# Performance work log

Hardware: AMD Instinct MI355X
Metric: run time of the kernel (lower is better)

The kernel has to match this reference:

```python
import jax, jax.numpy as jnp
from jax import lax
import numpy as np

D_MODEL = 256
NQ = 256          # nqueries / npoint
RADIUS = 0.3
NSAMPLE = 16
EPS = 1e-5


def _conv1d(x, W, b):  # x: (B,C,N), W: (O,C)
    return jnp.einsum('bcn,oc->bon', x, W) + b[None, :, None]


def _bn1d(x, g, be):  # train-mode batchnorm over (B, N)
    m = x.mean(axis=(0, 2), keepdims=True)
    v = x.var(axis=(0, 2), keepdims=True)
    return g[None, :, None] * (x - m) * lax.rsqrt(v + EPS) + be[None, :, None]


def _bn2d(x, g, be):  # x: (B,C,Q,S)
    m = x.mean(axis=(0, 2, 3), keepdims=True)
    v = x.var(axis=(0, 2, 3), keepdims=True)
    return g[None, :, None, None] * (x - m) * lax.rsqrt(v + EPS) + be[None, :, None, None]


def _fps(xyz, nq):
    # sequential farthest point sampling, starts at index 0 (matches CUDA impl)
    B, N, _ = xyz.shape

    def step(carry, _):
        dist, far = carry
        centroid = jnp.take_along_axis(xyz, far[:, None, None], axis=1)  # (B,1,3)
        d = jnp.sum((xyz - centroid) ** 2, axis=-1)                      # (B,N)
        dist = jnp.minimum(dist, d)
        nxt = jnp.argmax(dist, axis=-1).astype(jnp.int32)
        return (dist, nxt), far

    init = (jnp.full((B, N), 1e10, xyz.dtype), jnp.zeros((B,), jnp.int32))
    _, inds = lax.scan(step, init, None, length=nq)
    return inds.T  # (B,nq)


def _ball_query(query_xyz, xyz, radius, nsample):
    # query_xyz: (B,Q,3), xyz: (B,N,3) -> idx (B,Q,nsample) int32
    N = xyz.shape[1]
    d2 = jnp.sum((query_xyz[:, :, None, :] - xyz[:, None, :, :]) ** 2, axis=-1)  # (B,Q,N)
    within = d2 < radius * radius
    scores = jnp.where(within, jnp.arange(N, dtype=jnp.int32), jnp.int32(N))
    neg_top, _ = lax.top_k(-scores, nsample)          # nsample smallest scores, in order
    idx = -neg_top                                    # (B,Q,nsample)
    cnt = within.sum(axis=-1)                         # (B,Q)
    first = jnp.where(cnt > 0, idx[..., 0], 0)        # fill value (first neighbor, else 0)
    valid = jnp.arange(nsample) < cnt[..., None]
    return jnp.where(valid, idx, first[..., None])


def setup_inputs() -> dict:
    key = jax.random.key(0)
    ks = jax.random.split(key, 32)
    B, N, C = 16, 4096, D_MODEL
    s = 0.02
    inp = {
        'encode_xyz': jax.random.uniform(ks[0], (B, N, 3), jnp.float32),
        'encode_features': jax.random.normal(ks[1], (B, C, N), jnp.float32),
        # FFN_vote: conv1 -> bn -> relu -> conv2 -> bn -> relu -> conv3
        'W1': jax.random.normal(ks[2], (C, C), jnp.float32) * s,
        'b1': jnp.zeros((C,), jnp.float32),
        'g1': jnp.ones((C,), jnp.float32),
        'be1': jnp.zeros((C,), jnp.float32),
        'W2': jax.random.normal(ks[3], (C, C), jnp.float32) * s,
        'b2': jnp.zeros((C,), jnp.float32),
        'g2': jnp.ones((C,), jnp.float32),
        'be2': jnp.zeros((C,), jnp.float32),
        'W3': jax.random.normal(ks[4], (3 + C, C), jnp.float32) * s,
        'b3': jnp.zeros((3 + C,), jnp.float32),
        # SA module shared MLP (conv2d 1x1): (C+3)->C->C->C, each with BN2d
        'mW1': jax.random.normal(ks[5], (C, C + 3), jnp.float32) * s,
        'mb1': jnp.zeros((C,), jnp.float32),
        'mg1': jnp.ones((C,), jnp.float32),
        'mbe1': jnp.zeros((C,), jnp.float32),
        'mW2': jax.random.normal(ks[6], (C, C), jnp.float32) * s,
        'mb2': jnp.zeros((C,), jnp.float32),
        'mg2': jnp.ones((C,), jnp.float32),
        'mbe2': jnp.zeros((C,), jnp.float32),
        'mW3': jax.random.normal(ks[7], (C, C), jnp.float32) * s,
        'mb3': jnp.zeros((C,), jnp.float32),
        'mg3': jnp.ones((C,), jnp.float32),
        'mbe3': jnp.zeros((C,), jnp.float32),
    }
    return inp


def reference(encode_xyz, encode_features, W1, b1, g1, be1, W2, b2, g2, be2, W3, b3,
              mW1, mb1, mg1, mbe1, mW2, mb2, mg2, mbe2, mW3, mb3, mg3, mbe3):
    B, N, _ = encode_xyz.shape

    # FFN_vote
    h = jax.nn.relu(_bn1d(_conv1d(encode_features, W1, b1), g1, be1))
    h = jax.nn.relu(_bn1d(_conv1d(h, W2, b2), g2, be2))
    out = _conv1d(h, W3, b3)                      # (B, 3+C, N)

    coord_shift = jnp.clip(jax.nn.sigmoid(out[:, :3, :]), 0.1, 0.9)
    vote_xyz = encode_xyz + coord_shift.transpose(0, 2, 1) - 0.5   # (B,N,3)

    feat = encode_features + out[:, 3:, :]
    feat = feat / jnp.linalg.norm(feat, axis=1, keepdims=True)     # L2 normalize over C

    sample_inds = _fps(encode_xyz, NQ)                             # (B,NQ) int32

    # SA module: gather new centers from vote_xyz at FPS inds
    query_xyz = jnp.take_along_axis(vote_xyz, sample_inds[:, :, None], axis=1)  # (B,NQ,3)

    idx = _ball_query(query_xyz, vote_xyz, RADIUS, NSAMPLE)        # (B,NQ,NS)
    bidx = jnp.arange(B)[:, None, None]
    grouped_xyz = (vote_xyz[bidx, idx] - query_xyz[:, :, None, :]) / RADIUS  # (B,NQ,NS,3)
    grouped_feat = feat.transpose(0, 2, 1)[bidx, idx]                         # (B,NQ,NS,C)
    g = jnp.concatenate([grouped_xyz, grouped_feat], axis=-1)                 # (B,NQ,NS,3+C)
    g = g.transpose(0, 3, 1, 2)                                               # (B,3+C,NQ,NS)

    g = jax.nn.relu(_bn2d(jnp.einsum('bcqs,oc->boqs', g, mW1) + mb1[None, :, None, None], mg1, mbe1))
    g = jax.nn.relu(_bn2d(jnp.einsum('bcqs,oc->boqs', g, mW2) + mb2[None, :, None, None], mg2, mbe2))
    g = jax.nn.relu(_bn2d(jnp.einsum('bcqs,oc->boqs', g, mW3) + mb3[None, :, None, None], mg3, mbe3))
    query_features = jnp.max(g, axis=-1)                                      # (B,C,NQ)

    return vote_xyz, encode_xyz, sample_inds, query_xyz, query_features
```

## Files before the change

kernel.cpp:

```cpp
#include <hip/hip_runtime.h>
#include <math.h>

#define NPT 4096
#define NB 16

typedef short v8s __attribute__((ext_vector_type(8)));
typedef float v4f __attribute__((ext_vector_type(4)));

__device__ __forceinline__ float dist2e(float x, float y, float z,
                                        float cx, float cy, float cz) {
    float dx = __fsub_rn(x, cx), dy = __fsub_rn(y, cy), dz = __fsub_rn(z, cz);
    return __fadd_rn(__fadd_rn(__fmul_rn(dx, dx), __fmul_rn(dy, dy)), __fmul_rn(dz, dz));
}

__device__ __forceinline__ unsigned long long packdi(float v, int n) {
    return ((unsigned long long)__float_as_uint(v) << 32) |
           (unsigned long long)(0xFFFFFFFFu - (unsigned)n);
}

__device__ __forceinline__ unsigned short f2bf(float f) {
    unsigned u = __float_as_uint(f);
    u = u + 0x7FFFu + ((u >> 16) & 1u);
    return (unsigned short)(u >> 16);
}

__device__ __forceinline__ unsigned pk2(float a, float b) {
    unsigned r;
    asm("v_cvt_pk_bf16_f32 %0, %1, %2" : "=v"(r) : "v"(a), "v"(b));
    return r;
}

__device__ __forceinline__ uint2 split2(float a, float b) {
    unsigned h = pk2(a, b);
    float ra = __uint_as_float(h << 16);
    float rb = __uint_as_float(h & 0xFFFF0000u);
    unsigned l = pk2(a - ra, b - rb);
    return make_uint2(h, l);
}

__device__ void fps_seg(const float* __restrict__ xyz, int b, int it0, int it1,
                        int* __restrict__ inds_i, float* __restrict__ inds_f,
                        float* __restrict__ dws, int* __restrict__ farws,
                        char* scr) {
    float (*s_cent)[3] = (float (*)[3])scr;
    unsigned long long (*s_red)[4] = (unsigned long long (*)[4])(scr + 32);
    const int t = threadIdx.x;
    const int lane = t & 63, wid = t >> 6;
    const float* pb = xyz + (size_t)b * NPT * 3;
    float px[16], py[16], pz[16], d[16];
    #pragma unroll
    for (int j = 0; j < 16; ++j) {
        int p = j * 256 + t;
        px[j] = pb[p * 3 + 0];
        py[j] = pb[p * 3 + 1];
        pz[j] = pb[p * 3 + 2];
    }
    int far;
    if (it0 == 0) {
        #pragma unroll
        for (int j = 0; j < 16; ++j) d[j] = 1e10f;
        far = 0;
    } else {
        #pragma unroll
        for (int j = 0; j < 16; ++j) d[j] = dws[b * 4096 + j * 256 + t];
        far = farws[b];
    }
    for (int it = it0; it < it1; ++it) {
        const int par = it & 1;
        if (t == 0) { inds_i[it] = far; inds_f[it] = (float)far; }
        if (t == (far & 255)) {
            const int jj = far >> 8;
            float cx = px[0], cy = py[0], cz = pz[0];
            #pragma unroll
            for (int j = 1; j < 16; ++j)
                if (j == jj) { cx = px[j]; cy = py[j]; cz = pz[j]; }
            s_cent[par][0] = cx; s_cent[par][1] = cy; s_cent[par][2] = cz;
        }
        __syncthreads();
        const float cx = s_cent[par][0], cy = s_cent[par][1], cz = s_cent[par][2];
        d[0] = fminf(d[0], dist2e(px[0], py[0], pz[0], cx, cy, cz));
        unsigned long long best = packdi(d[0], t);
        #pragma unroll
        for (int j = 1; j < 16; ++j) {
            d[j] = fminf(d[j], dist2e(px[j], py[j], pz[j], cx, cy, cz));
            unsigned long long c = packdi(d[j], j * 256 + t);
            if (c > best) best = c;
        }
        #pragma unroll
        for (int s = 32; s; s >>= 1) {
            unsigned long long o = __shfl_down(best, (unsigned)s, 64);
            if (o > best) best = o;
        }
        if (lane == 0) s_red[par][wid] = best;
        __syncthreads();
        unsigned long long m = s_red[par][0];
        if (s_red[par][1] > m) m = s_red[par][1];
        if (s_red[par][2] > m) m = s_red[par][2];
        if (s_red[par][3] > m) m = s_red[par][3];
        far = (int)(0xFFFFFFFFu - (unsigned)(m & 0xFFFFFFFFull));
    }
    if (it1 < 256) {
        #pragma unroll
        for (int j = 0; j < 16; ++j) dws[b * 4096 + j * 256 + t] = d[j];
        if (t == 0) farws[b] = far;
    }
}

template <bool PRE_BN, bool STATS>
__global__ __launch_bounds__(256, 2)
void fgemm_k(const float* __restrict__ X,
             const unsigned short* __restrict__ Wh,
             const unsigned short* __restrict__ Wl,
             const float* __restrict__ bias,
             const float* __restrict__ scl, const float* __restrict__ sft,
             float* __restrict__ Y,
             float* __restrict__ psum, float* __restrict__ psqr,
             const float* __restrict__ xyz, int* __restrict__ sinds,
             float* __restrict__ inds_f, float* __restrict__ fpsd,
             int* __restrict__ fpsfar, int it0, int it1) {
    __shared__ __align__(16) unsigned short sAh[128 * 64];
    __shared__ __align__(16) unsigned short sAl[128 * 64];
    __shared__ __align__(16) unsigned short sBh[128 * 64];
    __shared__ __align__(16) unsigned short sBl[128 * 64];
    if (blockIdx.x < 16) {
        fps_seg(xyz, blockIdx.x, it0, it1, sinds + blockIdx.x * 256,
                inds_f + blockIdx.x * 256, fpsd, fpsfar, (char*)sAh);
        return;
    }
    int idx = blockIdx.x - 16;
    idx = (idx & 7) * 128 + (idx >> 3);
    const int b = idx >> 6, rem = idx & 63;
    const int nt = rem >> 1;
    const int n0 = nt * 128, o0 = (rem & 1) * 128;
    const int t = threadIdx.x;
    const int w = t >> 6, lane = t & 63;
    const int wm = (w >> 1) * 64, wn = (w & 1) * 64;
    const int lr = lane & 15, lk = lane >> 4;
    char* cAh = (char*)sAh; char* cAl = (char*)sAl;
    char* cBh = (char*)sBh; char* cBl = (char*)sBl;

    v4f acc[4][4];
    v4f zz = {0.f, 0.f, 0.f, 0.f};
    #pragma unroll
    for (int i = 0; i < 4; ++i)
        #pragma unroll
        for (int j = 0; j < 4; ++j) acc[i][j] = zz;

    const int ra = t >> 1, kb2 = (t & 1) * 64;
    const unsigned short* ah = Wh + (size_t)(o0 + ra) * 256 + (t & 1) * 32;
    const unsigned short* al = Wl + (size_t)(o0 + ra) * 256 + (t & 1) * 32;
    const int swA = (ra & 7) << 4;
    const int cblk = t >> 5, nq = t & 31;
    const float* xb = X + ((size_t)b * 256 + cblk * 8) * 4096 + n0 + nq * 4;

    #pragma unroll 1
    for (int ks = 0; ks < 4; ++ks) {
        const int k0 = ks * 64;
        uint4 avh[4], avl[4];
        #pragma unroll
        for (int i = 0; i < 4; ++i) {
            avh[i] = *(const uint4*)(ah + k0 + 8 * i);
            avl[i] = *(const uint4*)(al + k0 + 8 * i);
        }
        v4f xv[8];
        #pragma unroll
        for (int i = 0; i < 8; ++i)
            xv[i] = *(const v4f*)(xb + (size_t)(k0 + i) * 4096);
        if (PRE_BN) {
            const v4f s0 = *(const v4f*)(scl + k0 + cblk * 8);
            const v4f s1 = *(const v4f*)(scl + k0 + cblk * 8 + 4);
            const v4f f0 = *(const v4f*)(sft + k0 + cblk * 8);
            const v4f f1 = *(const v4f*)(sft + k0 + cblk * 8 + 4);
            #pragma unroll
            for (int i = 0; i < 8; ++i) {
                const float si = (i < 4) ? s0[i] : s1[i - 4];
                const float fi = (i < 4) ? f0[i] : f1[i - 4];
                #pragma unroll
                for (int j = 0; j < 4; ++j)
                    xv[i][j] = fmaxf(fmaf(xv[i][j], si, fi), 0.f);
            }
        }
        __syncthreads();
        #pragma unroll
        for (int i = 0; i < 4; ++i) {
            *(uint4*)(cAh + ra * 128 + ((kb2 + 16 * i) ^ swA)) = avh[i];
            *(uint4*)(cAl + ra * 128 + ((kb2 + 16 * i) ^ swA)) = avl[i];
        }
        #pragma unroll
        for (int j = 0; j < 4; ++j) {
            const int n = nq * 4 + j;
            uint2 p0 = split2(xv[0][j], xv[1][j]);
            uint2 p1 = split2(xv[2][j], xv[3][j]);
            uint2 p2 = split2(xv[4][j], xv[5][j]);
            uint2 p3 = split2(xv[6][j], xv[7][j]);
            uint4 hh, ll;
            hh.x = p0.x; hh.y = p1.x; hh.z = p2.x; hh.w = p3.x;
            ll.x = p0.y; ll.y = p1.y; ll.z = p2.y; ll.w = p3.y;
            const int ad = n * 128 + ((cblk * 16) ^ ((n & 7) << 4));
            *(uint4*)(cBh + ad) = hh;
            *(uint4*)(cBl + ad) = ll;
        }
        __syncthreads();
        #pragma unroll
        for (int kb = 0; kb < 2; ++kb) {
            const int koff = kb * 64 + lk * 16;
            v8s ahf[4], alf[4], bhf[4], blf[4];
            #pragma unroll
            for (int f = 0; f < 4; ++f) {
                const int rm = wm + f * 16 + lr;
                const int am = rm * 128 + (koff ^ ((rm & 7) << 4));
                ahf[f] = *(const v8s*)(cAh + am);
                alf[f] = *(const v8s*)(cAl + am);
                const int rn = wn + f * 16 + lr;
                const int bm = rn * 128 + (koff ^ ((rn & 7) << 4));
                bhf[f] = *(const v8s*)(cBh + bm);
                blf[f] = *(const v8s*)(cBl + bm);
            }
            #pragma unroll
            for (int fm = 0; fm < 4; ++fm)
                #pragma unroll
                for (int fn = 0; fn < 4; ++fn) {
                    acc[fm][fn] = __builtin_amdgcn_mfma_f32_16x16x32_bf16(
                        ahf[fm], bhf[fn], acc[fm][fn], 0, 0, 0);
                    acc[fm][fn] = __builtin_amdgcn_mfma_f32_16x16x32_bf16(
                        ahf[fm], blf[fn], acc[fm][fn], 0, 0, 0);
                    acc[fm][fn] = __builtin_amdgcn_mfma_f32_16x16x32_bf16(
                        alf[fm], bhf[fn], acc[fm][fn], 0, 0, 0);
                }
        }
    }

    float* Yb = Y + (size_t)b * 256 * 4096;
    const int gnt = b * 32 + nt;
    #pragma unroll
    for (int fm = 0; fm < 4; ++fm) {
        const int obase = o0 + wm + fm * 16 + lk * 4;
        float bv[4];
        #pragma unroll
        for (int j = 0; j < 4; ++j) bv[j] = bias[obase + j];
        float ssr[4] = {0.f, 0.f, 0.f, 0.f}, qqr[4] = {0.f, 0.f, 0.f, 0.f};
        #pragma unroll
        for (int fn = 0; fn < 4; ++fn) {
            const int gn = n0 + wn + fn * 16 + lr;
            #pragma unroll
            for (int j = 0; j < 4; ++j) {
                const float yv = acc[fm][fn][j] + bv[j];
                Yb[(size_t)(obase + j) * 4096 + gn] = yv;
                ssr[j] += yv; qqr[j] += yv * yv;
            }
        }
        if (STATS) {
            #pragma unroll
            for (int j = 0; j < 4; ++j) {
                #pragma unroll
                for (int off = 1; off < 16; off <<= 1) {
                    ssr[j] += __shfl_xor(ssr[j], off, 64);
                    qqr[j] += __shfl_xor(qqr[j], off, 64);
                }
            }
            if (lr == 0) {
                const int col = gnt * 2 + (w & 1);
                #pragma unroll
                for (int j = 0; j < 4; ++j) {
                    psum[(size_t)(obase + j) * 1024 + col] = ssr[j];
                    psqr[(size_t)(obase + j) * 1024 + col] = qqr[j];
                }
            }
        }
    }
}

__global__ __launch_bounds__(256)
void prepw_k(const float* __restrict__ W1, const float* __restrict__ W2,
             const float* __restrict__ W3, unsigned short* __restrict__ h1,
             unsigned short* __restrict__ l1, unsigned short* __restrict__ h2,
             unsigned short* __restrict__ l2, unsigned short* __restrict__ h3,
             unsigned short* __restrict__ l3) {
    const int o = blockIdx.x & 255, which = blockIdx.x >> 8, t = threadIdx.x;
    float v;
    unsigned short* ph;
    unsigned short* pl;
    if (which == 0) { v = W1[(size_t)o * 256 + t]; ph = h1; pl = l1; }
    else if (which == 1) { v = W2[(size_t)o * 256 + t]; ph = h2; pl = l2; }
    else { v = W3[(size_t)(o + 3) * 256 + t]; ph = h3; pl = l3; }
    unsigned short hu = f2bf(v);
    float rv = v - __uint_as_float((unsigned)hu << 16);
    ph[o * 256 + t] = hu;
    pl[o * 256 + t] = f2bf(rv);
}

__global__ __launch_bounds__(64)
void fin_k(const float* __restrict__ psum, const float* __restrict__ psqr,
           const float* __restrict__ g, const float* __restrict__ be,
           float* __restrict__ scl, float* __restrict__ sft, int npart) {
    const int c = blockIdx.x, t = threadIdx.x;
    const float4* ps = (const float4*)(psum + (size_t)c * 1024);
    const float4* pq = (const float4*)(psqr + (size_t)c * 1024);
    float s = 0.f, q = 0.f;
    for (int r = t; r < (npart >> 2); r += 64) {
        float4 a = ps[r]; s += a.x + a.y + a.z + a.w;
        float4 b2 = pq[r]; q += b2.x + b2.y + b2.z + b2.w;
    }
    #pragma unroll
    for (int sh = 32; sh; sh >>= 1) {
        s += __shfl_down(s, (unsigned)sh, 64);
        q += __shfl_down(q, (unsigned)sh, 64);
    }
    if (t == 0) {
        float mean = s * (1.f / 65536.f);
        float var = q * (1.f / 65536.f) - mean * mean;
        float sc = g[c] / sqrtf(var + 1e-5f);
        scl[c] = sc;
        sft[c] = be[c] - mean * sc;
    }
}

__global__ __launch_bounds__(256)
void prep_k(const float* __restrict__ mW1, const float* __restrict__ mW2,
            const float* __restrict__ mW3, unsigned short* __restrict__ W1p,
            unsigned short* __restrict__ W2p, unsigned short* __restrict__ W3p) {
    const int o = blockIdx.x & 255, which = blockIdx.x >> 8, t = threadIdx.x;
    if (which == 0) {
        W1p[o * 320 + t] = f2bf(mW1[o * 259 + 3 + t]);
        if (t < 64) {
            float v = (t < 3) ? mW1[o * 259 + t] : 0.f;
            W1p[o * 320 + 256 + t] = f2bf(v);
        }
    } else if (which == 1) {
        W2p[o * 256 + t] = f2bf(mW2[o * 256 + t]);
    } else {
        W3p[o * 256 + t] = f2bf(mW3[o * 256 + t]);
    }
}

__global__ __launch_bounds__(256)
void votefeat_k(const float* __restrict__ OUT, const float* __restrict__ Y2,
                const float* __restrict__ xyz, const float* __restrict__ feats,
                const float* __restrict__ scl2, const float* __restrict__ sft2,
                const float* __restrict__ W3, const float* __restrict__ b3,
                float* __restrict__ vote_out, float* __restrict__ xyz_out,
                unsigned short* __restrict__ featT) {
    const int blk = blockIdx.x;
    const int b = blk >> 7, n0 = (blk & 127) * 32;
    const int t = threadIdx.x;
    __shared__ float tile[32 * 257];
    __shared__ float ssb[32 * 9];
    __shared__ float rn[32];
    __shared__ float sW3[768];
    __shared__ float dred[3][8][33];
    const int nl = t & 31, co = t >> 5;
    const float* Ob = OUT + (size_t)b * 256 * NPT;
    const float* Yb = Y2 + (size_t)b * 256 * NPT;
    #pragma unroll
    for (int r = 0; r < 3; ++r) sW3[r * 256 + t] = W3[r * 256 + t];
    __syncthreads();
    float ss = 0.f, d0 = 0.f, d1 = 0.f, d2 = 0.f;
    #pragma unroll 4
    for (int ci = 0; ci < 32; ++ci) {
        const int c = ci * 8 + co;
        const size_t coff = (size_t)c * NPT + n0 + nl;
        float v = feats[(size_t)b * 256 * NPT + coff] + Ob[coff];
        tile[nl * 257 + c] = v;
        ss += v * v;
        float h = fmaxf(fmaf(Yb[coff], scl2[c], sft2[c]), 0.f);
        d0 = fmaf(h, sW3[c], d0);
        d1 = fmaf(h, sW3[256 + c], d1);
        d2 = fmaf(h, sW3[512 + c], d2);
    }
    ssb[nl * 9 + co] = ss;
    dred[0][co][nl] = d0;
    dred[1][co][nl] = d1;
    dred[2][co][nl] = d2;
    __syncthreads();
    if (t < 32) {
        float s = 0.f;
        #pragma unroll
        for (int j = 0; j < 8; ++j) s += ssb[t * 9 + j];
        rn[t] = 1.0f / sqrtf(s);
    }
    __syncthreads();
    for (int p = 0; p < 32; ++p)
        featT[((size_t)b * NPT + n0 + p) * 256 + t] = f2bf(tile[p * 257 + t] * rn[p]);
    if (t < 96) {
        const int r = t >> 5, p = t & 31;
        float d = b3[r];
        #pragma unroll
        for (int j = 0; j < 8; ++j) d += dred[r][j][p];
        float sig = 1.f / (1.f + expf(-d));
        sig = fminf(fmaxf(sig, 0.1f), 0.9f);
        const size_t gi = ((size_t)b * NPT + n0 + p) * 3 + r;
        const float e = xyz[gi];
        vote_out[gi] = e + sig - 0.5f;
        xyz_out[gi] = e;
    }
}

__global__ __launch_bounds__(64)
void bq_k(const float* __restrict__ vote, const int* __restrict__ sinds,
          float* __restrict__ qxyz_out, int* __restrict__ idx_out) {
    const int bq = blockIdx.x;
    const int b = bq >> 8;
    const int lane = threadIdx.x;
    __shared__ int s_idx[16];
    const int si = sinds[bq];
    const float* vb = vote + (size_t)b * NPT * 3;
    const float qx = vb[si * 3 + 0], qy = vb[si * 3 + 1], qz = vb[si * 3 + 2];
    if (lane < 3) qxyz_out[bq * 3 + lane] = vb[si * 3 + lane];
    int cnt = 0;
    for (int cb = 0; cb < 64 && cnt < 16; ++cb) {
        int n = cb * 64 + lane;
        float x = vb[n * 3], y = vb[n * 3 + 1], z = vb[n * 3 + 2];
        float d2 = dist2e(x, y, z, qx, qy, qz);
        unsigned long long m = __ballot(d2 < 0.09f);
        while (m && cnt < 16) {
            int bit = __builtin_ctzll(m);
            s_idx[cnt] = cb * 64 + bit;
            ++cnt;
            m &= m - 1;
        }
    }
    __syncthreads();
    if (lane < 16) {
        int v = (lane < cnt) ? s_idx[lane] : (cnt > 0 ? s_idx[0] : 0);
        idx_out[bq * 16 + lane] = v;
    }
}

__global__ __launch_bounds__(256)
void group_k(const unsigned short* __restrict__ featT, const float* __restrict__ vote,
             const float* __restrict__ qxyz, const int* __restrict__ idxs,
             unsigned short* __restrict__ Gt) {
    const int bq = blockIdx.x;
    const int b = bq >> 8, q = bq & 255;
    const int t = threadIdx.x;
    __shared__ int s_i[16];
    __shared__ float s_q[3];
    if (t < 16) s_i[t] = idxs[bq * 16 + t];
    if (t < 3) s_q[t] = qxyz[bq * 3 + t];
    __syncthreads();
    const int s = t >> 4, part = t & 15;
    const int i = s_i[s];
    const size_t nrow = (size_t)b * 4096 + q * 16 + s;
    const uint4* src = (const uint4*)(featT + ((size_t)b * NPT + i) * 256 + part * 16);
    uint4* dst = (uint4*)(Gt + nrow * 320 + part * 16);
    dst[0] = src[0];
    dst[1] = src[1];
    for (int c = 259 + part; c < 320; c += 16) Gt[nrow * 320 + c] = 0;
    if (part < 3) {
        float v = (vote[((size_t)b * NPT + i) * 3 + part] - s_q[part]) * (1.f / 0.3f);
        Gt[nrow * 320 + 256 + part] = f2bf(v);
    }
}

__device__ __forceinline__ unsigned bnpair(unsigned u, float sl, float sh,
                                           float fl, float fh) {
    float lo = __uint_as_float(u << 16);
    float hi = __uint_as_float(u & 0xFFFF0000u);
    lo = fmaxf(fmaf(lo, sl, fl), 0.f);
    hi = fmaxf(fmaf(hi, sh, fh), 0.f);
    unsigned r;
    asm("v_cvt_pk_bf16_f32 %0, %1, %2" : "=v"(r) : "v"(lo), "v"(hi));
    return r;
}

template <int KPAD, bool BNSTAGE, bool EPIMAX>
__global__ __launch_bounds__(256, 2)
void mgemm_k(const unsigned short* __restrict__ Wb,
             const unsigned short* __restrict__ Xt,
             const float* __restrict__ bias,
             const float* __restrict__ scl, const float* __restrict__ sft,
             unsigned short* __restrict__ Yt, float* __restrict__ rmax,
             float* __restrict__ psum, float* __restrict__ psqr) {
    __shared__ __align__(16) unsigned short sA[128 * 64];
    __shared__ __align__(16) unsigned short sB[128 * 64];
    char* cA = (char*)sA;
    char* cB = (char*)sB;
    const int t = threadIdx.x;
    const int n0 = blockIdx.x * 128, o0 = blockIdx.y * 128;
    const int w = t >> 6, lane = t & 63;
    const int wm = (w >> 1) * 64, wn = (w & 1) * 64;
    const int lr = lane & 15, lk = lane >> 4;

    v4f acc[4][4];
    v4f zz = {0.f, 0.f, 0.f, 0.f};
    #pragma unroll
    for (int i = 0; i < 4; ++i)
        #pragma unroll
        for (int j = 0; j < 4; ++j) acc[i][j] = zz;

    const int ra = t >> 1, kc = (t & 1) * 32;
    const unsigned short* asrc = Wb + (size_t)(o0 + ra) * KPAD + kc;
    const unsigned short* bsrc = Xt + (size_t)(n0 + ra) * KPAD + kc;
    const int nk = KPAD / 64;

    for (int ks = 0; ks < nk; ++ks) {
        const int k0 = ks * 64;
        uint4 av[4], bv[4];
        #pragma unroll
        for (int i = 0; i < 4; ++i) av[i] = *(const uint4*)(asrc + k0 + 8 * i);
        #pragma unroll
        for (int i = 0; i < 4; ++i) bv[i] = *(const uint4*)(bsrc + k0 + 8 * i);
        if constexpr (BNSTAGE) {
            #pragma unroll
            for (int i = 0; i < 4; ++i) {
                const int kk = k0 + kc + 8 * i;
                float4 s0 = *(const float4*)(scl + kk);
                float4 s1 = *(const float4*)(scl + kk + 4);
                float4 f0 = *(const float4*)(sft + kk);
                float4 f1 = *(const float4*)(sft + kk + 4);
                bv[i].x = bnpair(bv[i].x, s0.x, s0.y, f0.x, f0.y);
                bv[i].y = bnpair(bv[i].y, s0.z, s0.w, f0.z, f0.w);
                bv[i].z = bnpair(bv[i].z, s1.x, s1.y, f1.x, f1.y);
                bv[i].w = bnpair(bv[i].w, s1.z, s1.w, f1.z, f1.w);
            }
        }
        __syncthreads();
        #pragma unroll
        for (int i = 0; i < 4; ++i) {
            const int kb2 = (kc + 8 * i) * 2;
            *(uint4*)(cA + ra * 128 + (kb2 ^ ((ra & 7) << 4))) = av[i];
            *(uint4*)(cB + ra * 128 + (kb2 ^ ((ra & 7) << 4))) = bv[i];
        }
        __syncthreads();
        #pragma unroll
        for (int kb = 0; kb < 2; ++kb) {
            const int koff = (kb * 32 + lk * 8) * 2;
            v8s af[4], bf[4];
            #pragma unroll
            for (int f = 0; f < 4; ++f) {
                const int rm = wm + f * 16 + lr;
                af[f] = *(const v8s*)(cA + rm * 128 + (koff ^ ((rm & 7) << 4)));
                const int rn = wn + f * 16 + lr;
                bf[f] = *(const v8s*)(cB + rn * 128 + (koff ^ ((rn & 7) << 4)));
            }
            #pragma unroll
            for (int fm = 0; fm < 4; ++fm)
                #pragma unroll
                for (int fn = 0; fn < 4; ++fn)
                    acc[fm][fn] = __builtin_amdgcn_mfma_f32_16x16x32_bf16(
                        af[fm], bf[fn], acc[fm][fn], 0, 0, 0);
        }
    }

    const int bx = blockIdx.x;
    #pragma unroll
    for (int fm = 0; fm < 4; ++fm) {
        const int obase = o0 + wm + fm * 16 + lk * 4;
        const float4 bv4 = *(const float4*)(bias + obase);
        float s0 = 0.f, s1 = 0.f, s2 = 0.f, s3 = 0.f;
        float q0 = 0.f, q1 = 0.f, q2 = 0.f, q3 = 0.f;
        #pragma unroll
        for (int fn = 0; fn < 4; ++fn) {
            float y0 = acc[fm][fn][0] + bv4.x;
            float y1 = acc[fm][fn][1] + bv4.y;
            float y2 = acc[fm][fn][2] + bv4.z;
            float y3 = acc[fm][fn][3] + bv4.w;
            s0 += y0; s1 += y1; s2 += y2; s3 += y3;
            q0 += y0 * y0; q1 += y1 * y1; q2 += y2 * y2; q3 += y3 * y3;
            if constexpr (!EPIMAX) {
                unsigned p0, p1;
                asm("v_cvt_pk_bf16_f32 %0, %1, %2" : "=v"(p0) : "v"(y0), "v"(y1));
                asm("v_cvt_pk_bf16_f32 %0, %1, %2" : "=v"(p1) : "v"(y2), "v"(y3));
                const int gn = n0 + wn + fn * 16 + lr;
                *(uint2*)(Yt + (size_t)gn * 256 + obase) = make_uint2(p0, p1);
            } else {
                float m0 = y0, m1 = y1, m2 = y2, m3 = y3;
                #pragma unroll
                for (int off = 1; off < 16; off <<= 1) {
                    m0 = fmaxf(m0, __shfl_xor(m0, off, 64));
                    m1 = fmaxf(m1, __shfl_xor(m1, off, 64));
                    m2 = fmaxf(m2, __shfl_xor(m2, off, 64));
                    m3 = fmaxf(m3, __shfl_xor(m3, off, 64));
                }
                if (lr == 0) {
                    const int gq = (n0 + wn + fn * 16) >> 4;
                    const int bb = gq >> 8, qq = gq & 255;
                    float* rp = rmax + ((size_t)bb * 256 + obase) * 256 + qq;
                    rp[0] = m0; rp[256] = m1; rp[512] = m2; rp[768] = m3;
                }
            }
        }
        #pragma unroll
        for (int off = 1; off < 16; off <<= 1) {
            s0 += __shfl_xor(s0, off, 64); q0 += __shfl_xor(q0, off, 64);
            s1 += __shfl_xor(s1, off, 64); q1 += __shfl_xor(q1, off, 64);
            s2 += __shfl_xor(s2, off, 64); q2 += __shfl_xor(q2, off, 64);
            s3 += __shfl_xor(s3, off, 64); q3 += __shfl_xor(q3, off, 64);
        }
        if (lr == 0) {
            const int col = bx * 2 + (w & 1);
            psum[(size_t)(obase + 0) * 1024 + col] = s0;
            psum[(size_t)(obase + 1) * 1024 + col] = s1;
            psum[(size_t)(obase + 2) * 1024 + col] = s2;
            psum[(size_t)(obase + 3) * 1024 + col] = s3;
            psqr[(size_t)(obase + 0) * 1024 + col] = q0;
            psqr[(size_t)(obase + 1) * 1024 + col] = q1;
            psqr[(size_t)(obase + 2) * 1024 + col] = q2;
            psqr[(size_t)(obase + 3) * 1024 + col] = q3;
        }
    }
}

__global__ __launch_bounds__(256)
void qf_k(const float* __restrict__ rmax, const float* __restrict__ scl,
          const float* __restrict__ sft, float* __restrict__ out) {
    const int g = blockIdx.x * 256 + threadIdx.x;
    const int c = (g >> 8) & 255;
    out[g] = fmaxf(fmaf(rmax[g], scl[c], sft[c]), 0.f);
}

extern "C" void kernel_launch(void* const* d_in, const int* in_sizes, int n_in,
                              void* d_out, int out_size, void* d_ws, size_t ws_size,
                              hipStream_t stream) {
    const float* xyz   = (const float*)d_in[0];
    const float* feats = (const float*)d_in[1];
    const float* W1 = (const float*)d_in[2];
    const float* b1 = (const float*)d_in[3];
    const float* g1 = (const float*)d_in[4];
    const float* be1 = (const float*)d_in[5];
    const float* W2 = (const float*)d_in[6];
    const float* b2 = (const float*)d_in[7];
    const float* g2 = (const float*)d_in[8];
    const float* be2 = (const float*)d_in[9];
    const float* W3 = (const float*)d_in[10];
    const float* b3 = (const float*)d_in[11];
    const float* mW1 = (const float*)d_in[12];
    const float* mb1 = (const float*)d_in[13];
    const float* mg1 = (const float*)d_in[14];
    const float* mbe1 = (const float*)d_in[15];
    const float* mW2 = (const float*)d_in[16];
    const float* mb2 = (const float*)d_in[17];
    const float* mg2 = (const float*)d_in[18];
    const float* mbe2 = (const float*)d_in[19];
    const float* mW3 = (const float*)d_in[20];
    const float* mb3 = (const float*)d_in[21];
    const float* mg3 = (const float*)d_in[22];
    const float* mbe3 = (const float*)d_in[23];

    float* out_vote = (float*)d_out;
    float* out_xyz = out_vote + 196608;
    float* out_inds = out_xyz + 196608;
    float* out_q = out_inds + 4096;
    float* out_qf = out_q + 12288;

    float* ws = (float*)d_ws;
    float* A      = ws;
    float* Bb     = A + 16973824;
    float* Ft     = Bb + 16777216;
    float* rawmax = Ft + 8388608;
    float* psum   = rawmax + 1048576;
    float* psqr   = psum + 262144;
    float* st     = psqr + 262144;
    float* fpsd   = st + 2560;
    float* wbase  = fpsd + 65536;
    unsigned short* Wb1 = (unsigned short*)wbase;
    unsigned short* Wb2 = Wb1 + 81920;
    unsigned short* Wb3 = Wb2 + 65536;
    int* sinds  = (int*)(Wb3 + 65536);
    int* bidx   = sinds + 4096;
    int* fpsfar = bidx + 65536;

    unsigned short* Gt  = (unsigned short*)A;
    unsigned short* Y1t = (unsigned short*)Bb;
    unsigned short* featT = (unsigned short*)Ft;
    unsigned short* Y2t = (unsigned short*)Ft;

    unsigned short* Wf1h = (unsigned short*)rawmax;
    unsigned short* Wf1l = Wf1h + 65536;
    unsigned short* Wf2h = Wf1l + 65536;
    unsigned short* Wf2l = Wf2h + 65536;
    unsigned short* Wf3h = Wf2l + 65536;
    unsigned short* Wf3l = Wf3h + 65536;

    prep_k<<<768, 256, 0, stream>>>(mW1, mW2, mW3, Wb1, Wb2, Wb3);
    prepw_k<<<768, 256, 0, stream>>>(W1, W2, W3, Wf1h, Wf1l, Wf2h, Wf2l, Wf3h, Wf3l);

    fgemm_k<false, true><<<1040, 256, 0, stream>>>(
        feats, Wf1h, Wf1l, b1, nullptr, nullptr, A, psum, psqr,
        xyz, sinds, out_inds, fpsd, fpsfar, 0, 86);
    fin_k<<<256, 64, 0, stream>>>(psum, psqr, g1, be1, st + 0, st + 256, 1024);
    fgemm_k<true, true><<<1040, 256, 0, stream>>>(
        A, Wf2h, Wf2l, b2, st + 0, st + 256, Bb, psum, psqr,
        xyz, sinds, out_inds, fpsd, fpsfar, 86, 172);
    fin_k<<<256, 64, 0, stream>>>(psum, psqr, g2, be2, st + 512, st + 768, 1024);
    fgemm_k<true, false><<<1040, 256, 0, stream>>>(
        Bb, Wf3h, Wf3l, b3 + 3, st + 512, st + 768, A, nullptr, nullptr,
        xyz, sinds, out_inds, fpsd, fpsfar, 172, 256);

    votefeat_k<<<2048, 256, 0, stream>>>(A, Bb, xyz, feats, st + 512, st + 768,
                                         W3, b3, out_vote, out_xyz, featT);
    bq_k<<<4096, 64, 0, stream>>>(out_vote, sinds, out_q, bidx);
    group_k<<<4096, 256, 0, stream>>>(featT, out_vote, out_q, bidx, Gt);

    mgemm_k<320, false, false><<<dim3(512, 2), 256, 0, stream>>>(
        Wb1, Gt, mb1, nullptr, nullptr, Y1t, nullptr, psum, psqr);
    fin_k<<<256, 64, 0, stream>>>(psum, psqr, mg1, mbe1, st + 1024, st + 1280, 1024);
    mgemm_k<256, true, false><<<dim3(512, 2), 256, 0, stream>>>(
        Wb2, Y1t, mb2, st + 1024, st + 1280, Y2t, nullptr, psum, psqr);
    fin_k<<<256, 64, 0, stream>>>(psum, psqr, mg2, mbe2, st + 1536, st + 1792, 1024);
    mgemm_k<256, true, true><<<dim3(512, 2), 256, 0, stream>>>(
        Wb3, Y2t, mb3, st + 1536, st + 1792, nullptr, rawmax, psum, psqr);
    fin_k<<<256, 64, 0, stream>>>(psum, psqr, mg3, mbe3, st + 2048, st + 2304, 1024);
    qf_k<<<4096, 256, 0, stream>>>(rawmax, st + 2048, st + 2304, out_qf);
}
```

Measured before the change: 609.8 us.

## Rebalance FPS across four kernels, DPP reductions, drop A-tile LDS staging

```diff
diff --git a/kernel.cpp b/kernel.cpp
--- a/kernel.cpp
+++ b/kernel.cpp
@@ -38,12 +38,24 @@
     return make_uint2(h, l);
 }
 
+template <int CTRL>
+__device__ __forceinline__ float dpp_maxf(float v) {
+    int o = __builtin_amdgcn_update_dpp(__float_as_int(v), __float_as_int(v),
+                                        CTRL, 0xF, 0xF, false);
+    return fmaxf(v, __int_as_float(o));
+}
+template <int CTRL>
+__device__ __forceinline__ unsigned dpp_maxu(unsigned v) {
+    unsigned o = (unsigned)__builtin_amdgcn_update_dpp((int)v, (int)v,
+                                                       CTRL, 0xF, 0xF, false);
+    return v > o ? v : o;
+}
+
 __device__ void fps_seg(const float* __restrict__ xyz, int b, int it0, int it1,
                         int* __restrict__ inds_i, float* __restrict__ inds_f,
                         float* __restrict__ dws, int* __restrict__ farws,
                         char* scr) {
-    float (*s_cent)[3] = (float (*)[3])scr;
-    unsigned long long (*s_red)[4] = (unsigned long long (*)[4])(scr + 32);
+    unsigned long long (*s_red)[4] = (unsigned long long (*)[4])scr;
     const int t = threadIdx.x;
     const int lane = t & 63, wid = t >> 6;
     const float* pb = xyz + (size_t)b * NPT * 3;
@@ -68,16 +80,9 @@
     for (int it = it0; it < it1; ++it) {
         const int par = it & 1;
         if (t == 0) { inds_i[it] = far; inds_f[it] = (float)far; }
-        if (t == (far & 255)) {
-            const int jj = far >> 8;
-            float cx = px[0], cy = py[0], cz = pz[0];
-            #pragma unroll
-            for (int j = 1; j < 16; ++j)
-                if (j == jj) { cx = px[j]; cy = py[j]; cz = pz[j]; }
-            s_cent[par][0] = cx; s_cent[par][1] = cy; s_cent[par][2] = cz;
-        }
-        __syncthreads();
-        const float cx = s_cent[par][0], cy = s_cent[par][1], cz = s_cent[par][2];
+        const float cx = pb[far * 3 + 0];
+        const float cy = pb[far * 3 + 1];
+        const float cz = pb[far * 3 + 2];
         d[0] = fminf(d[0], dist2e(px[0], py[0], pz[0], cx, cy, cz));
         unsigned long long best = packdi(d[0], t);
         #pragma unroll
@@ -86,18 +91,32 @@
             unsigned long long c = packdi(d[j], j * 256 + t);
             if (c > best) best = c;
         }
-        #pragma unroll
-        for (int s = 32; s; s >>= 1) {
-            unsigned long long o = __shfl_down(best, (unsigned)s, 64);
-            if (o > best) best = o;
-        }
-        if (lane == 0) s_red[par][wid] = best;
+        const unsigned hi = (unsigned)(best >> 32);
+        const unsigned lo = (unsigned)(best & 0xFFFFFFFFull);
+        float m = __uint_as_float(hi);
+        m = dpp_maxf<0x111>(m);
+        m = dpp_maxf<0x112>(m);
+        m = dpp_maxf<0x114>(m);
+        m = dpp_maxf<0x118>(m);
+        m = dpp_maxf<0x142>(m);
+        m = dpp_maxf<0x143>(m);
+        const unsigned mbits = (unsigned)__builtin_amdgcn_readlane(__float_as_int(m), 63);
+        unsigned cand = (hi == mbits) ? lo : 0u;
+        cand = dpp_maxu<0x111>(cand);
+        cand = dpp_maxu<0x112>(cand);
+        cand = dpp_maxu<0x114>(cand);
+        cand = dpp_maxu<0x118>(cand);
+        cand = dpp_maxu<0x142>(cand);
+        cand = dpp_maxu<0x143>(cand);
+        const unsigned wlo = (unsigned)__builtin_amdgcn_readlane((int)cand, 63);
+        if (lane == 0)
+            s_red[par][wid] = ((unsigned long long)mbits << 32) | (unsigned long long)wlo;
         __syncthreads();
-        unsigned long long m = s_red[par][0];
-        if (s_red[par][1] > m) m = s_red[par][1];
-        if (s_red[par][2] > m) m = s_red[par][2];
-        if (s_red[par][3] > m) m = s_red[par][3];
-        far = (int)(0xFFFFFFFFu - (unsigned)(m & 0xFFFFFFFFull));
+        unsigned long long mm = s_red[par][0];
+        if (s_red[par][1] > mm) mm = s_red[par][1];
+        if (s_red[par][2] > mm) mm = s_red[par][2];
+        if (s_red[par][3] > mm) mm = s_red[par][3];
+        far = (int)(0xFFFFFFFFu - (unsigned)(mm & 0xFFFFFFFFull));
     }
     if (it1 < 256) {
         #pragma unroll
@@ -107,7 +126,7 @@
 }
 
 template <bool PRE_BN, bool STATS>
-__global__ __launch_bounds__(256, 2)
+__global__ __launch_bounds__(256, 4)
 void fgemm_k(const float* __restrict__ X,
              const unsigned short* __restrict__ Wh,
              const unsigned short* __restrict__ Wl,
@@ -118,13 +137,11 @@
              const float* __restrict__ xyz, int* __restrict__ sinds,
              float* __restrict__ inds_f, float* __restrict__ fpsd,
              int* __restrict__ fpsfar, int it0, int it1) {
-    __shared__ __align__(16) unsigned short sAh[128 * 64];
-    __shared__ __align__(16) unsigned short sAl[128 * 64];
     __shared__ __align__(16) unsigned short sBh[128 * 64];
     __shared__ __align__(16) unsigned short sBl[128 * 64];
     if (blockIdx.x < 16) {
         fps_seg(xyz, blockIdx.x, it0, it1, sinds + blockIdx.x * 256,
-                inds_f + blockIdx.x * 256, fpsd, fpsfar, (char*)sAh);
+                inds_f + blockIdx.x * 256, fpsd, fpsfar, (char*)sBh);
         return;
     }
     int idx = blockIdx.x - 16;
@@ -136,8 +153,8 @@
     const int w = t >> 6, lane = t & 63;
     const int wm = (w >> 1) * 64, wn = (w & 1) * 64;
     const int lr = lane & 15, lk = lane >> 4;
-    char* cAh = (char*)sAh; char* cAl = (char*)sAl;
-    char* cBh = (char*)sBh; char* cBl = (char*)sBl;
+    char* cBh = (char*)sBh;
+    char* cBl = (char*)sBl;
 
     v4f acc[4][4];
     v4f zz = {0.f, 0.f, 0.f, 0.f};
@@ -146,22 +163,16 @@
         #pragma unroll
         for (int j = 0; j < 4; ++j) acc[i][j] = zz;
 
-    const int ra = t >> 1, kb2 = (t & 1) * 64;
-    const unsigned short* ah = Wh + (size_t)(o0 + ra) * 256 + (t & 1) * 32;
-    const unsigned short* al = Wl + (size_t)(o0 + ra) * 256 + (t & 1) * 32;
-    const int swA = (ra & 7) << 4;
+    const size_t aoff = (size_t)(o0 + wm + lr) * 256 + lk * 8;
+    const unsigned short* pah = Wh + aoff;
+    const unsigned short* pal = Wl + aoff;
+
     const int cblk = t >> 5, nq = t & 31;
     const float* xb = X + ((size_t)b * 256 + cblk * 8) * 4096 + n0 + nq * 4;
 
     #pragma unroll 1
     for (int ks = 0; ks < 4; ++ks) {
         const int k0 = ks * 64;
-        uint4 avh[4], avl[4];
-        #pragma unroll
-        for (int i = 0; i < 4; ++i) {
-            avh[i] = *(const uint4*)(ah + k0 + 8 * i);
-            avl[i] = *(const uint4*)(al + k0 + 8 * i);
-        }
         v4f xv[8];
         #pragma unroll
         for (int i = 0; i < 8; ++i)
@@ -182,11 +193,6 @@
         }
         __syncthreads();
         #pragma unroll
-        for (int i = 0; i < 4; ++i) {
-            *(uint4*)(cAh + ra * 128 + ((kb2 + 16 * i) ^ swA)) = avh[i];
-            *(uint4*)(cAl + ra * 128 + ((kb2 + 16 * i) ^ swA)) = avl[i];
-        }
-        #pragma unroll
         for (int j = 0; j < 4; ++j) {
             const int n = nq * 4 + j;
             uint2 p0 = split2(xv[0][j], xv[1][j]);
@@ -204,13 +210,12 @@
         #pragma unroll
         for (int kb = 0; kb < 2; ++kb) {
             const int koff = kb * 64 + lk * 16;
+            const int ka = k0 + kb * 32;
             v8s ahf[4], alf[4], bhf[4], blf[4];
             #pragma unroll
             for (int f = 0; f < 4; ++f) {
-                const int rm = wm + f * 16 + lr;
-                const int am = rm * 128 + (koff ^ ((rm & 7) << 4));
-                ahf[f] = *(const v8s*)(cAh + am);
-                alf[f] = *(const v8s*)(cAl + am);
+                ahf[f] = *(const v8s*)(pah + (size_t)f * 4096 + ka);
+                alf[f] = *(const v8s*)(pal + (size_t)f * 4096 + ka);
                 const int rn = wn + f * 16 + lr;
                 const int bm = rn * 128 + (koff ^ ((rn & 7) << 4));
                 bhf[f] = *(const v8s*)(cBh + bm);
@@ -339,15 +344,23 @@
                 const float* __restrict__ scl2, const float* __restrict__ sft2,
                 const float* __restrict__ W3, const float* __restrict__ b3,
                 float* __restrict__ vote_out, float* __restrict__ xyz_out,
-                unsigned short* __restrict__ featT) {
-    const int blk = blockIdx.x;
-    const int b = blk >> 7, n0 = (blk & 127) * 32;
-    const int t = threadIdx.x;
+                unsigned short* __restrict__ featT,
+                int* __restrict__ sinds, float* __restrict__ inds_f,
+                float* __restrict__ fpsd, int* __restrict__ fpsfar,
+                int it0, int it1) {
     __shared__ float tile[32 * 257];
     __shared__ float ssb[32 * 9];
     __shared__ float rn[32];
     __shared__ float sW3[768];
     __shared__ float dred[3][8][33];
+    if (blockIdx.x < 16) {
+        fps_seg(xyz, blockIdx.x, it0, it1, sinds + blockIdx.x * 256,
+                inds_f + blockIdx.x * 256, fpsd, fpsfar, (char*)tile);
+        return;
+    }
+    const int blk = blockIdx.x - 16;
+    const int b = blk >> 7, n0 = (blk & 127) * 32;
+    const int t = threadIdx.x;
     const int nl = t & 31, co = t >> 5;
     const float* Ob = OUT + (size_t)b * 256 * NPT;
     const float* Yb = Y2 + (size_t)b * 256 * NPT;
@@ -677,18 +690,19 @@
 
     fgemm_k<false, true><<<1040, 256, 0, stream>>>(
         feats, Wf1h, Wf1l, b1, nullptr, nullptr, A, psum, psqr,
-        xyz, sinds, out_inds, fpsd, fpsfar, 0, 86);
+        xyz, sinds, out_inds, fpsd, fpsfar, 0, 64);
     fin_k<<<256, 64, 0, stream>>>(psum, psqr, g1, be1, st + 0, st + 256, 1024);
     fgemm_k<true, true><<<1040, 256, 0, stream>>>(
         A, Wf2h, Wf2l, b2, st + 0, st + 256, Bb, psum, psqr,
-        xyz, sinds, out_inds, fpsd, fpsfar, 86, 172);
+        xyz, sinds, out_inds, fpsd, fpsfar, 64, 128);
     fin_k<<<256, 64, 0, stream>>>(psum, psqr, g2, be2, st + 512, st + 768, 1024);
     fgemm_k<true, false><<<1040, 256, 0, stream>>>(
         Bb, Wf3h, Wf3l, b3 + 3, st + 512, st + 768, A, nullptr, nullptr,
-        xyz, sinds, out_inds, fpsd, fpsfar, 172, 256);
-
-    votefeat_k<<<2048, 256, 0, stream>>>(A, Bb, xyz, feats, st + 512, st + 768,
-                                         W3, b3, out_vote, out_xyz, featT);
+        xyz, sinds, out_inds, fpsd, fpsfar, 128, 192);
+
+    votefeat_k<<<2064, 256, 0, stream>>>(A, Bb, xyz, feats, st + 512, st + 768,
+                                         W3, b3, out_vote, out_xyz, featT,
+                                         sinds, out_inds, fpsd, fpsfar, 192, 256);
     bq_k<<<4096, 64, 0, stream>>>(out_vote, sinds, out_q, bidx);
     group_k<<<4096, 256, 0, stream>>>(featT, out_vote, out_q, bidx, Gt);
 
```

Result: faster. 565.0 us (-7.3%).
